# Kernel tuning notes

Measured on AMD Instinct MI355X. Metric: run time of the kernel, lower is better.

## Reference

```python
import jax, jax.numpy as jnp
import numpy as np

N_TOKEN = 256
C_PAIR = 128
C = 32
N_HEADS = 4
LN_EPS = 1e-5


def setup_inputs() -> dict:
    key = jax.random.key(0)
    ks = jax.random.split(key, 8)
    w = lambda k, shape: jax.random.normal(k, shape, dtype=jnp.float32) * 0.02
    return {
        "pair": jax.random.normal(ks[0], (N_TOKEN, N_TOKEN, C_PAIR), dtype=jnp.float32),
        "gamma": jnp.ones((C_PAIR,), dtype=jnp.float32),
        "beta": jnp.zeros((C_PAIR,), dtype=jnp.float32),
        "Wq": w(ks[1], (C_PAIR, C * N_HEADS)),
        "Wk": w(ks[2], (C_PAIR, C * N_HEADS)),
        "Wv": w(ks[3], (C_PAIR, C * N_HEADS)),
        "Wb": w(ks[4], (C_PAIR, N_HEADS)),
        "Wg": w(ks[5], (C_PAIR, C * N_HEADS)),
        "Wout": w(ks[6], (C * N_HEADS, C_PAIR)),
    }


def _layernorm(x, gamma, beta):
    mu = jnp.mean(x, axis=-1, keepdims=True)
    var = jnp.mean(jnp.square(x - mu), axis=-1, keepdims=True)
    return (x - mu) * jax.lax.rsqrt(var + LN_EPS) * gamma + beta


def reference(pair, gamma, beta, Wq, Wk, Wv, Wb, Wg, Wout):
    n = pair.shape[0]
    pn = _layernorm(pair, gamma, beta)  # [N, N, c_pair]
    q = (pn @ Wq).reshape(n, n, N_HEADS, C)  # [i, j, h, c]
    k = (pn @ Wk).reshape(n, n, N_HEADS, C)  # [i, k, h, c]
    v = (pn @ Wv).reshape(n, n, N_HEADS, C)
    b = pn @ Wb                               # [j, k, h] pairwise bias
    g = jax.nn.sigmoid(pn @ Wg).reshape(n, n, N_HEADS, C)
    # a^h_ijk = softmax_k( q_ij . k_ik / sqrt(c) + b_jk )
    logits = jnp.einsum("ijhc,ikhc->ijkh", q, k) / np.float32(np.sqrt(C))
    logits = logits + b[None, :, :, :]        # broadcast over i: bias indexed by (j, k)
    attn = jax.nn.softmax(logits, axis=2)     # softmax over k axis
    o = jnp.einsum("ijkh,ikhc->ijhc", attn, v) * g
    return o.reshape(n, n, N_HEADS * C) @ Wout  # [N, N, c_pair]
```

## Files before the change

### kernel.cpp

```cpp
#include <hip/hip_runtime.h>

#define N_TOK 256
#define CP    128
#define CHD   32
#define NH    4
#define NT    65536
#define NCOL  528

typedef short short8 __attribute__((ext_vector_type(8)));
typedef float f32x4  __attribute__((ext_vector_type(4)));

__device__ __forceinline__ short f2bf(float f) {
    unsigned u = __builtin_bit_cast(unsigned, f);
    u += 0x7fffu + ((u >> 16) & 1u);
    return (short)(u >> 16);
}
__device__ __forceinline__ float bf2f(short s) {
    unsigned u = ((unsigned)(unsigned short)s) << 16;
    return __builtin_bit_cast(float, u);
}

__global__ void pack_weights(const float* __restrict__ Wq, const float* __restrict__ Wk,
                             const float* __restrict__ Wv, const float* __restrict__ Wb,
                             const float* __restrict__ Wg, const float* __restrict__ Wout,
                             short* __restrict__ wcat, short* __restrict__ woutT) {
    int idx = blockIdx.x * 256 + threadIdx.x;
    if (idx < NCOL * CP) {
        int n = idx >> 7, k = idx & 127;
        float v = 0.f;
        if (n < 512) {
            const float* W = (n < 128) ? Wq : (n < 256) ? Wk : (n < 384) ? Wv : Wg;
            int col = (n & 96) + 2 * (n & 15) + ((n >> 4) & 1);
            v = W[k * 128 + col];
            if (n < 128) v *= 0.17677669529663687f;
        } else if (n < 516) {
            v = Wb[k * 4 + (n - 512)];
        }
        wcat[n * CP + k] = f2bf(v);
    } else {
        int j = idx - NCOL * CP;
        if (j < 128 * 128) {
            int n = j >> 7, k = j & 127;
            woutT[n * 128 + k] = f2bf(Wout[k * 128 + n]);
        }
    }
}

__global__ __launch_bounds__(256, 4)
void ln_proj(const float* __restrict__ pair, const float* __restrict__ gamma,
             const float* __restrict__ beta, const short* __restrict__ wcat,
             short* __restrict__ qt, short* __restrict__ kt,
             short* __restrict__ vt, short* __restrict__ gt,
             float* __restrict__ bt) {
    __shared__ short pn[64 * 136];
    const int tid = threadIdx.x;
    const int wv = tid >> 6, lane = tid & 63;
    const int quad = lane >> 4, l15 = lane & 15;
    const int r0 = blockIdx.x * 64;

    float ga0 = gamma[2 * lane], ga1 = gamma[2 * lane + 1];
    float be0 = beta[2 * lane],  be1 = beta[2 * lane + 1];

    #pragma unroll 4
    for (int rr = 0; rr < 16; ++rr) {
        int row = wv * 16 + rr;
        const float* src = pair + (size_t)(r0 + row) * CP + 2 * lane;
        float x0 = src[0], x1 = src[1];
        float s = x0 + x1;
        #pragma unroll
        for (int m = 32; m; m >>= 1) s += __shfl_xor(s, m);
        float mu = s * (1.f / 128.f);
        float d0 = x0 - mu, d1 = x1 - mu;
        float vs = d0 * d0 + d1 * d1;
        #pragma unroll
        for (int m = 32; m; m >>= 1) vs += __shfl_xor(vs, m);
        float rs = rsqrtf(vs * (1.f / 128.f) + 1e-5f);
        short y0 = f2bf(d0 * rs * ga0 + be0);
        short y1 = f2bf(d1 * rs * ga1 + be1);
        unsigned pk = ((unsigned)(unsigned short)y0) | (((unsigned)(unsigned short)y1) << 16);
        *(unsigned*)&pn[row * 136 + 2 * lane] = pk;
    }
    __syncthreads();

    short8 af[4][4];
    #pragma unroll
    for (int rt = 0; rt < 4; ++rt)
        #pragma unroll
        for (int s = 0; s < 4; ++s)
            af[rt][s] = *(const short8*)&pn[(rt * 16 + l15) * 136 + s * 32 + quad * 8];

    short* const dst = (wv == 0) ? qt : (wv == 1) ? kt : (wv == 2) ? vt : gt;

#define LOADB(BUF, CHN) {                                                          \
        int n_ = (CHN) * 16 + l15;                                                 \
        _Pragma("unroll")                                                          \
        for (int s = 0; s < 4; ++s)                                                \
            BUF[s] = *(const short8*)&wcat[(size_t)n_ * CP + s * 32 + quad * 8];   \
    }

#define EVEN(BUF) {                                                                \
        _Pragma("unroll")                                                          \
        for (int rt = 0; rt < 4; ++rt) {                                           \
            f32x4 a = {0.f, 0.f, 0.f, 0.f};                                        \
            _Pragma("unroll")                                                      \
            for (int s = 0; s < 4; ++s)                                            \
                a = __builtin_amdgcn_mfma_f32_16x16x32_bf16(af[rt][s], BUF[s], a, 0, 0, 0); \
            accE[rt] = a;                                                          \
        }                                                                          \
    }

#define ODD(CC, BUF) {                                                             \
        const int chn = wv * 8 + (CC);                                             \
        const int h_ = (chn >> 1) & 3;                                             \
        const size_t hb = (size_t)h_ * NT * CHD + 2 * l15;                         \
        _Pragma("unroll")                                                          \
        for (int rt = 0; rt < 4; ++rt) {                                           \
            f32x4 a = {0.f, 0.f, 0.f, 0.f};                                        \
            _Pragma("unroll")                                                      \
            for (int s = 0; s < 4; ++s)                                            \
                a = __builtin_amdgcn_mfma_f32_16x16x32_bf16(af[rt][s], BUF[s], a, 0, 0, 0); \
            _Pragma("unroll")                                                      \
            for (int r = 0; r < 4; ++r) {                                          \
                int gr = r0 + rt * 16 + quad * 4 + r;                              \
                float ve = accE[rt][r], vo = a[r];                                 \
                if (wv == 3) {                                                     \
                    ve = 1.f / (1.f + __expf(-ve));                                \
                    vo = 1.f / (1.f + __expf(-vo));                                \
                }                                                                  \
                unsigned pk = ((unsigned)(unsigned short)f2bf(ve))                 \
                            | (((unsigned)(unsigned short)f2bf(vo)) << 16);        \
                *(unsigned*)&dst[hb + (size_t)gr * CHD] = pk;                      \
            }                                                                      \
        }                                                                          \
    }

    short8 bA[4], bB[4];
    f32x4 accE[4];
    LOADB(bA, wv * 8 + 0)
    LOADB(bB, wv * 8 + 1)
    EVEN(bA) LOADB(bA, wv * 8 + 2)
    ODD(1, bB) LOADB(bB, wv * 8 + 3)
    EVEN(bA) LOADB(bA, wv * 8 + 4)
    ODD(3, bB) LOADB(bB, wv * 8 + 5)
    EVEN(bA) LOADB(bA, wv * 8 + 6)
    ODD(5, bB) LOADB(bB, wv * 8 + 7)
    EVEN(bA) LOADB(bA, wv * 8 + 8)
    ODD(7, bB)

    if (wv == 3) {
        #pragma unroll
        for (int rt = 0; rt < 4; ++rt) {
            f32x4 acc = {0.f, 0.f, 0.f, 0.f};
            #pragma unroll
            for (int s = 0; s < 4; ++s)
                acc = __builtin_amdgcn_mfma_f32_16x16x32_bf16(af[rt][s], bA[s], acc, 0, 0, 0);
            if (l15 < 4) {
                #pragma unroll
                for (int r = 0; r < 4; ++r) {
                    int gr = r0 + rt * 16 + quad * 4 + r;
                    bt[l15 * NT + gr] = acc[r];
                }
            }
        }
    }
#undef LOADB
#undef EVEN
#undef ODD
}

__global__ __launch_bounds__(256)
void attn(const short* __restrict__ qt, const short* __restrict__ kt,
          const short* __restrict__ vt, const short* __restrict__ gt,
          const float* __restrict__ bt, short* __restrict__ og) {
    __shared__ short vT[32 * 264];
    __shared__ short pl[64 * 264];
    const int tid = threadIdx.x;
    const int h = blockIdx.x >> 8, i = blockIdx.x & 255;
    const int wv = tid >> 6, lane = tid & 63;
    const int quad = lane >> 4, l15 = lane & 15;

    const short* kbase = kt + ((size_t)h * NT + (size_t)i * 256) * CHD;
    const short* vbase = vt + ((size_t)h * NT + (size_t)i * 256) * CHD;
    const short* qbase = qt + ((size_t)h * NT + (size_t)i * 256) * CHD;
    const short* gbase = gt + ((size_t)h * NT + (size_t)i * 256) * CHD;
    const float* bbase = bt + (size_t)h * NT;

    for (int g = tid; g < 1024; g += 256) {
        int key = g >> 2, p = g & 3;
        short8 s = *(const short8*)(vbase + key * CHD + p * 8);
        #pragma unroll
        for (int cc = 0; cc < 8; ++cc) {
            int c = p * 8 + cc;
            int row = (c & 1) ? 16 + (c >> 1) : (c >> 1);
            vT[row * 264 + key] = s[cc];
        }
    }
    __syncthreads();

    for (int jt = 0; jt < 4; ++jt) {
        int jbase = jt * 64 + wv * 16;
        short8 aq = *(const short8*)(qbase + (jbase + l15) * CHD + quad * 8);

        f32x4 sacc[16];
        __builtin_amdgcn_s_setprio(1);
        #pragma unroll
        for (int t = 0; t < 16; ++t) {
            f32x4 c;
            #pragma unroll
            for (int r = 0; r < 4; ++r)
                c[r] = bbase[(size_t)(jbase + quad * 4 + r) * 256 + t * 16 + l15];
            short8 bk = *(const short8*)(kbase + (t * 16 + l15) * CHD + quad * 8);
            sacc[t] = __builtin_amdgcn_mfma_f32_16x16x32_bf16(aq, bk, c, 0, 0, 0);
        }
        __builtin_amdgcn_s_setprio(0);
        float mx[4] = {-1e30f, -1e30f, -1e30f, -1e30f}, sm[4] = {0.f, 0.f, 0.f, 0.f};
        #pragma unroll
        for (int t = 0; t < 16; ++t)
            #pragma unroll
            for (int r = 0; r < 4; ++r) mx[r] = fmaxf(mx[r], sacc[t][r]);
        #pragma unroll
        for (int m = 1; m < 16; m <<= 1)
            #pragma unroll
            for (int r = 0; r < 4; ++r) mx[r] = fmaxf(mx[r], __shfl_xor(mx[r], m, 16));
        #pragma unroll
        for (int t = 0; t < 16; ++t)
            #pragma unroll
            for (int r = 0; r < 4; ++r) {
                float e = __expf(sacc[t][r] - mx[r]);
                sacc[t][r] = e;
                sm[r] += e;
            }
        #pragma unroll
        for (int m = 1; m < 16; m <<= 1)
            #pragma unroll
            for (int r = 0; r < 4; ++r) sm[r] += __shfl_xor(sm[r], m, 16);
        float inv[4];
        #pragma unroll
        for (int r = 0; r < 4; ++r) inv[r] = 1.f / sm[r];
        #pragma unroll
        for (int t = 0; t < 16; ++t)
            #pragma unroll
            for (int r = 0; r < 4; ++r)
                pl[(wv * 16 + quad * 4 + r) * 264 + t * 16 + l15] = f2bf(sacc[t][r] * inv[r]);
        f32x4 oacc[2];
        oacc[0] = f32x4{0.f, 0.f, 0.f, 0.f};
        oacc[1] = f32x4{0.f, 0.f, 0.f, 0.f};
        __builtin_amdgcn_s_setprio(1);
        #pragma unroll
        for (int ks = 0; ks < 8; ++ks) {
            short8 ap = *(const short8*)&pl[(wv * 16 + l15) * 264 + ks * 32 + quad * 8];
            #pragma unroll
            for (int nt = 0; nt < 2; ++nt) {
                short8 bv = *(const short8*)&vT[(nt * 16 + l15) * 264 + ks * 32 + quad * 8];
                oacc[nt] = __builtin_amdgcn_mfma_f32_16x16x32_bf16(ap, bv, oacc[nt], 0, 0, 0);
            }
        }
        __builtin_amdgcn_s_setprio(0);
        #pragma unroll
        for (int r = 0; r < 4; ++r) {
            int j = jbase + quad * 4 + r;
            unsigned gw = *(const unsigned*)(gbase + (size_t)j * CHD + 2 * l15);
            float g0 = bf2f((short)(gw & 0xffff));
            float g1 = bf2f((short)(gw >> 16));
            unsigned pk = ((unsigned)(unsigned short)f2bf(oacc[0][r] * g0))
                        | (((unsigned)(unsigned short)f2bf(oacc[1][r] * g1)) << 16);
            *(unsigned*)&og[((size_t)i * 256 + j) * CP + h * CHD + 2 * l15] = pk;
        }
    }
}

__global__ __launch_bounds__(256)
void out_gemm(const short* __restrict__ og, const short* __restrict__ woutT,
              float* __restrict__ out) {
    __shared__ short al[64 * 136];
    const int tid = threadIdx.x;
    const int wv = tid >> 6, lane = tid & 63;
    const int quad = lane >> 4, l15 = lane & 15;
    const int r0 = blockIdx.x * 64;

    for (int g = tid; g < 1024; g += 256) {
        int row = g >> 4, p = g & 15;
        *(short8*)&al[row * 136 + p * 8] = *(const short8*)(og + (size_t)(r0 + row) * CP + p * 8);
    }
    __syncthreads();

    short8 af[4];
    #pragma unroll
    for (int s = 0; s < 4; ++s)
        af[s] = *(const short8*)&al[(wv * 16 + l15) * 136 + s * 32 + quad * 8];

    #pragma unroll
    for (int ch = 0; ch < 8; ++ch) {
        int n = ch * 16 + l15;
        f32x4 acc = {0.f, 0.f, 0.f, 0.f};
        #pragma unroll
        for (int s = 0; s < 4; ++s) {
            short8 bfrag = *(const short8*)&woutT[(size_t)n * 128 + s * 32 + quad * 8];
            acc = __builtin_amdgcn_mfma_f32_16x16x32_bf16(af[s], bfrag, acc, 0, 0, 0);
        }
        #pragma unroll
        for (int r = 0; r < 4; ++r)
            out[(size_t)(r0 + wv * 16 + quad * 4 + r) * CP + n] = acc[r];
    }
}

extern "C" void kernel_launch(void* const* d_in, const int* in_sizes, int n_in,
                              void* d_out, int out_size, void* d_ws, size_t ws_size,
                              hipStream_t stream) {
    (void)in_sizes; (void)n_in; (void)out_size; (void)ws_size;
    const float* pair  = (const float*)d_in[0];
    const float* gamma = (const float*)d_in[1];
    const float* beta  = (const float*)d_in[2];
    const float* Wq    = (const float*)d_in[3];
    const float* Wk    = (const float*)d_in[4];
    const float* Wv    = (const float*)d_in[5];
    const float* Wb    = (const float*)d_in[6];
    const float* Wg    = (const float*)d_in[7];
    const float* Wout  = (const float*)d_in[8];
    float* out = (float*)d_out;

    char* ws = (char*)d_ws;
    const size_t SZ_QKVG = (size_t)NH * NT * CHD * 2;
    short* wcat  = (short*)(ws);
    short* woutT = (short*)(ws + 135168);
    short* qt    = (short*)(ws + 167936);
    short* kt    = (short*)(ws + 167936 + SZ_QKVG);
    short* vt    = (short*)(ws + 167936 + 2 * SZ_QKVG);
    short* gt    = (short*)(ws + 167936 + 3 * SZ_QKVG);
    float* bt    = (float*)(ws + 167936 + 4 * SZ_QKVG);
    short* og    = (short*)(ws + 167936 + 4 * SZ_QKVG + (size_t)NH * NT * 4);

    hipLaunchKernelGGL(pack_weights, dim3(328), dim3(256), 0, stream,
                       Wq, Wk, Wv, Wb, Wg, Wout, wcat, woutT);
    hipLaunchKernelGGL(ln_proj, dim3(1024), dim3(256), 0, stream,
                       pair, gamma, beta, wcat, qt, kt, vt, gt, bt);
    hipLaunchKernelGGL(attn, dim3(1024), dim3(256), 0, stream,
                       qt, kt, vt, gt, bt, og);
    hipLaunchKernelGGL(out_gemm, dim3(1024), dim3(256), 0, stream,
                       og, woutT, out);
}
```

Measured before the change: 206.2 us.

## Coalesce projection stores, pre-transpose pair bias, and widen output GEMM stores

The Q/K/V/G projection outputs are now staged through per-wave shared memory and written back as contiguous 16-byte rows instead of scattered 4-byte stores. A new small kernel transposes the pair bias so the attention kernel can load each bias fragment as one vector instead of four strided scalar loads. The output GEMM permutes Wout columns so each lane computes two adjacent output columns, which lets it keep weights in registers and issue paired float stores. In exchange there is an extra kernel launch, an extra bias buffer, an added barrier, and more shared memory in ln_proj.

```diff
diff --git a/kernel.cpp b/kernel.cpp
--- a/kernel.cpp
+++ b/kernel.cpp
@@ -9,6 +9,7 @@
 
 typedef short short8 __attribute__((ext_vector_type(8)));
 typedef float f32x4  __attribute__((ext_vector_type(4)));
+typedef float f32x2  __attribute__((ext_vector_type(2)));
 
 __device__ __forceinline__ short f2bf(float f) {
     unsigned u = __builtin_bit_cast(unsigned, f);
@@ -41,7 +42,8 @@
         int j = idx - NCOL * CP;
         if (j < 128 * 128) {
             int n = j >> 7, k = j & 127;
-            woutT[n * 128 + k] = f2bf(Wout[k * 128 + n]);
+            int col = (n & 96) + 2 * (n & 15) + ((n >> 4) & 1);
+            woutT[n * 128 + k] = f2bf(Wout[k * 128 + col]);
         }
     }
 }
@@ -52,11 +54,12 @@
              short* __restrict__ qt, short* __restrict__ kt,
              short* __restrict__ vt, short* __restrict__ gt,
              float* __restrict__ bt) {
-    __shared__ short pn[64 * 136];
+    __shared__ short pn[10240];
     const int tid = threadIdx.x;
     const int wv = tid >> 6, lane = tid & 63;
     const int quad = lane >> 4, l15 = lane & 15;
     const int r0 = blockIdx.x * 64;
+    short* const ST = &pn[wv * 2560];
 
     float ga0 = gamma[2 * lane], ga1 = gamma[2 * lane + 1];
     float be0 = beta[2 * lane],  be1 = beta[2 * lane + 1];
@@ -88,6 +91,7 @@
         #pragma unroll
         for (int s = 0; s < 4; ++s)
             af[rt][s] = *(const short8*)&pn[(rt * 16 + l15) * 136 + s * 32 + quad * 8];
+    __syncthreads();
 
     short* const dst = (wv == 0) ? qt : (wv == 1) ? kt : (wv == 2) ? vt : gt;
 
@@ -112,7 +116,6 @@
 #define ODD(CC, BUF) {                                                             \
         const int chn = wv * 8 + (CC);                                             \
         const int h_ = (chn >> 1) & 3;                                             \
-        const size_t hb = (size_t)h_ * NT * CHD + 2 * l15;                         \
         _Pragma("unroll")                                                          \
         for (int rt = 0; rt < 4; ++rt) {                                           \
             f32x4 a = {0.f, 0.f, 0.f, 0.f};                                        \
@@ -121,7 +124,7 @@
                 a = __builtin_amdgcn_mfma_f32_16x16x32_bf16(af[rt][s], BUF[s], a, 0, 0, 0); \
             _Pragma("unroll")                                                      \
             for (int r = 0; r < 4; ++r) {                                          \
-                int gr = r0 + rt * 16 + quad * 4 + r;                              \
+                int rowl = rt * 16 + quad * 4 + r;                                 \
                 float ve = accE[rt][r], vo = a[r];                                 \
                 if (wv == 3) {                                                     \
                     ve = 1.f / (1.f + __expf(-ve));                                \
@@ -129,8 +132,16 @@
                 }                                                                  \
                 unsigned pk = ((unsigned)(unsigned short)f2bf(ve))                 \
                             | (((unsigned)(unsigned short)f2bf(vo)) << 16);        \
-                *(unsigned*)&dst[hb + (size_t)gr * CHD] = pk;                      \
+                *(unsigned*)&ST[rowl * 40 + 2 * l15] = pk;                         \
             }                                                                      \
+        }                                                                          \
+        const size_t hb2 = (size_t)h_ * NT * CHD + (size_t)r0 * CHD;               \
+        _Pragma("unroll")                                                          \
+        for (int s = 0; s < 4; ++s) {                                              \
+            int f = s * 64 + lane;                                                 \
+            int row = f >> 2, cs = (f & 3) * 8;                                    \
+            short8 v = *(const short8*)&ST[row * 40 + cs];                         \
+            *(short8*)(dst + hb2 + (size_t)row * CHD + cs) = v;                    \
         }                                                                          \
     }
 
@@ -169,9 +180,30 @@
 }
 
 __global__ __launch_bounds__(256)
+void bias_T(const float* __restrict__ bt, float* __restrict__ btT) {
+    __shared__ float t[64][65];
+    int bid = blockIdx.x;
+    int h = bid >> 4, tj = (bid >> 2) & 3, tk = bid & 3;
+    const float* src = bt + (size_t)h * NT;
+    float* dstp = btT + (size_t)h * NT;
+    int c = threadIdx.x & 63, r4 = threadIdx.x >> 6;
+    #pragma unroll
+    for (int rr = 0; rr < 16; ++rr) {
+        int r = rr * 4 + r4;
+        t[r][c] = src[(size_t)(tj * 64 + r) * 256 + tk * 64 + c];
+    }
+    __syncthreads();
+    #pragma unroll
+    for (int rr = 0; rr < 16; ++rr) {
+        int k = rr * 4 + r4;
+        dstp[(size_t)(tk * 64 + k) * 256 + tj * 64 + c] = t[c][k];
+    }
+}
+
+__global__ __launch_bounds__(256)
 void attn(const short* __restrict__ qt, const short* __restrict__ kt,
           const short* __restrict__ vt, const short* __restrict__ gt,
-          const float* __restrict__ bt, short* __restrict__ og) {
+          const float* __restrict__ btT, short* __restrict__ og) {
     __shared__ short vT[32 * 264];
     __shared__ short pl[64 * 264];
     const int tid = threadIdx.x;
@@ -183,7 +215,7 @@
     const short* vbase = vt + ((size_t)h * NT + (size_t)i * 256) * CHD;
     const short* qbase = qt + ((size_t)h * NT + (size_t)i * 256) * CHD;
     const short* gbase = gt + ((size_t)h * NT + (size_t)i * 256) * CHD;
-    const float* bbase = bt + (size_t)h * NT;
+    const float* btTb = btT + (size_t)h * NT;
 
     for (int g = tid; g < 1024; g += 256) {
         int key = g >> 2, p = g & 3;
@@ -205,10 +237,7 @@
         __builtin_amdgcn_s_setprio(1);
         #pragma unroll
         for (int t = 0; t < 16; ++t) {
-            f32x4 c;
-            #pragma unroll
-            for (int r = 0; r < 4; ++r)
-                c[r] = bbase[(size_t)(jbase + quad * 4 + r) * 256 + t * 16 + l15];
+            f32x4 c = *(const f32x4*)(btTb + (size_t)(t * 16 + l15) * 256 + jbase + quad * 4);
             short8 bk = *(const short8*)(kbase + (t * 16 + l15) * CHD + quad * 8);
             sacc[t] = __builtin_amdgcn_mfma_f32_16x16x32_bf16(aq, bk, c, 0, 0, 0);
         }
@@ -284,23 +313,33 @@
     }
     __syncthreads();
 
-    short8 af[4];
-    #pragma unroll
-    for (int s = 0; s < 4; ++s)
-        af[s] = *(const short8*)&al[(wv * 16 + l15) * 136 + s * 32 + quad * 8];
-
-    #pragma unroll
-    for (int ch = 0; ch < 8; ++ch) {
-        int n = ch * 16 + l15;
-        f32x4 acc = {0.f, 0.f, 0.f, 0.f};
+    short8 af[4][4];
+    #pragma unroll
+    for (int rt = 0; rt < 4; ++rt)
+        #pragma unroll
+        for (int s = 0; s < 4; ++s)
+            af[rt][s] = *(const short8*)&al[(rt * 16 + l15) * 136 + s * 32 + quad * 8];
+
+    short8 bE[4], bO[4];
+    #pragma unroll
+    for (int s = 0; s < 4; ++s) {
+        bE[s] = *(const short8*)&woutT[(size_t)(wv * 32 + l15) * 128 + s * 32 + quad * 8];
+        bO[s] = *(const short8*)&woutT[(size_t)(wv * 32 + 16 + l15) * 128 + s * 32 + quad * 8];
+    }
+
+    #pragma unroll
+    for (int rt = 0; rt < 4; ++rt) {
+        f32x4 accE = {0.f, 0.f, 0.f, 0.f}, accO = {0.f, 0.f, 0.f, 0.f};
         #pragma unroll
         for (int s = 0; s < 4; ++s) {
-            short8 bfrag = *(const short8*)&woutT[(size_t)n * 128 + s * 32 + quad * 8];
-            acc = __builtin_amdgcn_mfma_f32_16x16x32_bf16(af[s], bfrag, acc, 0, 0, 0);
-        }
-        #pragma unroll
-        for (int r = 0; r < 4; ++r)
-            out[(size_t)(r0 + wv * 16 + quad * 4 + r) * CP + n] = acc[r];
+            accE = __builtin_amdgcn_mfma_f32_16x16x32_bf16(af[rt][s], bE[s], accE, 0, 0, 0);
+            accO = __builtin_amdgcn_mfma_f32_16x16x32_bf16(af[rt][s], bO[s], accO, 0, 0, 0);
+        }
+        #pragma unroll
+        for (int r = 0; r < 4; ++r) {
+            f32x2 pk = {accE[r], accO[r]};
+            *(f32x2*)&out[(size_t)(r0 + rt * 16 + quad * 4 + r) * CP + wv * 32 + 2 * l15] = pk;
+        }
     }
 }
 
@@ -328,14 +367,16 @@
     short* vt    = (short*)(ws + 167936 + 2 * SZ_QKVG);
     short* gt    = (short*)(ws + 167936 + 3 * SZ_QKVG);
     float* bt    = (float*)(ws + 167936 + 4 * SZ_QKVG);
-    short* og    = (short*)(ws + 167936 + 4 * SZ_QKVG + (size_t)NH * NT * 4);
+    float* btT   = (float*)(ws + 167936 + 4 * SZ_QKVG + (size_t)NH * NT * 4);
+    short* og    = (short*)(ws + 167936 + 4 * SZ_QKVG + 2 * (size_t)NH * NT * 4);
 
     hipLaunchKernelGGL(pack_weights, dim3(328), dim3(256), 0, stream,
                        Wq, Wk, Wv, Wb, Wg, Wout, wcat, woutT);
     hipLaunchKernelGGL(ln_proj, dim3(1024), dim3(256), 0, stream,
                        pair, gamma, beta, wcat, qt, kt, vt, gt, bt);
+    hipLaunchKernelGGL(bias_T, dim3(64), dim3(256), 0, stream, bt, btT);
     hipLaunchKernelGGL(attn, dim3(1024), dim3(256), 0, stream,
-                       qt, kt, vt, gt, bt, og);
+                       qt, kt, vt, gt, btT, og);
     hipLaunchKernelGGL(out_gemm, dim3(1024), dim3(256), 0, stream,
                        og, woutT, out);
 }
```

Measured after the change: 195.9 us. -5.0%, faster.
